# Performance work log

Hardware: AMD Instinct MI355X
Metric: run time of the kernel (lower is better)

The kernel has to match this reference:

```python
import jax, jax.numpy as jnp
import numpy as np

B, T, H = 4096, 2048, 15  # batch, seq_len, n_hidden (hardcoded 15 in module)


def setup_inputs() -> dict:
    key = jax.random.key(0)
    ks = jax.random.split(key, 7)
    s = 1.0 / np.sqrt(H)  # torch default init scale for LSTMCell/Linear
    return {
        "x": jax.random.normal(ks[0], (B, T), dtype=jnp.float32),
        "W_ih": jax.random.uniform(ks[1], (4 * H, 1), jnp.float32, -s, s),
        "W_hh": jax.random.uniform(ks[2], (4 * H, H), jnp.float32, -s, s),
        "b_ih": jax.random.uniform(ks[3], (4 * H,), jnp.float32, -s, s),
        "b_hh": jax.random.uniform(ks[4], (4 * H,), jnp.float32, -s, s),
        "W_lin": jax.random.uniform(ks[5], (1, H), jnp.float32, -s, s),
        "b_lin": jax.random.uniform(ks[6], (1,), jnp.float32, -s, s),
    }


def reference(x, W_ih, W_hh, b_ih, b_hh, W_lin, b_lin):
    # x: [B, T]; one scalar input per timestep (LSTMCell input_size=1).
    b = b_ih + b_hh  # [4H]
    w_ih = W_ih[:, 0]  # [4H] since input_size == 1

    def step(carry, x_t):
        h, c = carry  # [B, H] each
        # gates: [B, 4H], PyTorch gate order i, f, g, o
        gates = x_t[:, None] * w_ih[None, :] + h @ W_hh.T + b
        i_, f_, g_, o_ = jnp.split(gates, 4, axis=1)
        c = jax.nn.sigmoid(f_) * c + jax.nn.sigmoid(i_) * jnp.tanh(g_)
        h = jax.nn.sigmoid(o_) * jnp.tanh(c)
        out = h @ W_lin.T + b_lin  # [B, 1]
        return (h, c), out[:, 0]

    h0 = jnp.zeros((x.shape[0], W_hh.shape[1]), x.dtype)
    c0 = jnp.zeros_like(h0)
    _, outs = jax.lax.scan(step, (h0, c0), x.T)  # outs: [T, B]
    return outs.T  # [B, T], matches torch.cat(outputs, dim=1)
```

## Files before the change

kernel.cpp:

```cpp
#include <hip/hip_runtime.h>


#define HID 15
#define T_LEN 2048
#define B_TOT 4096

template<int CTRL>
__device__ __forceinline__ int dpp_i(int v) {
    return __builtin_amdgcn_update_dpp(0, v, CTRL, 0xF, 0xF, true);
}
template<int CTRL>
__device__ __forceinline__ float dpp_f(float v) {
    return __int_as_float(
        __builtin_amdgcn_update_dpp(0, __float_as_int(v), CTRL, 0xF, 0xF, true));
}

__global__ __launch_bounds__(256) __attribute__((amdgpu_waves_per_eu(1, 1)))
void lstm_seq_kernel(
    const float* __restrict__ x,
    const float* __restrict__ W_ih,
    const float* __restrict__ W_hh,
    const float* __restrict__ b_ih,
    const float* __restrict__ b_hh,
    const float* __restrict__ W_lin,
    const float* __restrict__ b_lin,
    float* __restrict__ out)
{
    const int tid = threadIdx.x;
    const int sub = tid & 15;
    const int u   = (sub < HID) ? sub : (HID - 1);
    const int b   = blockIdx.x * 16 + (tid >> 4);

    int pos[16];
    pos[0]  = sub;
    pos[1]  = dpp_i<0x121>(sub);  pos[2]  = dpp_i<0x122>(sub);
    pos[3]  = dpp_i<0x123>(sub);  pos[4]  = dpp_i<0x124>(sub);
    pos[5]  = dpp_i<0x125>(sub);  pos[6]  = dpp_i<0x126>(sub);
    pos[7]  = dpp_i<0x127>(sub);  pos[8]  = dpp_i<0x128>(sub);
    pos[9]  = dpp_i<0x129>(sub);  pos[10] = dpp_i<0x12A>(sub);
    pos[11] = dpp_i<0x12B>(sub);  pos[12] = dpp_i<0x12C>(sub);
    pos[13] = dpp_i<0x12D>(sub);  pos[14] = dpp_i<0x12E>(sub);
    pos[15] = dpp_i<0x12F>(sub);

    const int r0 = u, r1 = HID + u, r2 = 2 * HID + u, r3 = 3 * HID + u;
    float wg0[16], wg1[16], wg2[16], wg3[16];
#pragma unroll
    for (int j = 0; j < 16; ++j) {
        const int p = pos[j];
        const bool v = (p < HID);
        wg0[j] = v ? W_hh[r0 * HID + p] : 0.0f;
        wg1[j] = v ? W_hh[r1 * HID + p] : 0.0f;
        wg2[j] = v ? W_hh[r2 * HID + p] : 0.0f;
        wg3[j] = v ? W_hh[r3 * HID + p] : 0.0f;
    }
    const float wih0 = W_ih[r0], wih1 = W_ih[r1], wih2 = W_ih[r2], wih3 = W_ih[r3];
    const float bi0 = b_ih[r0] + b_hh[r0];
    const float bi1 = b_ih[r1] + b_hh[r1];
    const float bi2 = b_ih[r2] + b_hh[r2];
    const float bi3 = b_ih[r3] + b_hh[r3];
    const float wlin_m = (sub < HID) ? W_lin[sub] : 0.0f;
    const float blin = b_lin[0];

    const float L  = 1.44269504088896341f;

    float c = 0.0f, hl = 0.0f;
    const float4* __restrict__ x4 = (const float4*)(x + (size_t)b * T_LEN);
    float4* __restrict__ o4       = (float4*)(out + (size_t)b * T_LEN);

    float4 xv = x4[0];
    for (int t0 = 0; t0 < T_LEN / 4; ++t0) {
        const int tn = (t0 + 1 < T_LEN / 4) ? (t0 + 1) : t0;
        const float4 xnext = x4[tn];
        float ov[4];
#pragma unroll
        for (int s = 0; s < 4; ++s) {
            const float xt = (s == 0) ? xv.x : (s == 1) ? xv.y : (s == 2) ? xv.z : xv.w;

            float hr[16];
            hr[0]  = hl;
            hr[1]  = dpp_f<0x121>(hl);  hr[2]  = dpp_f<0x122>(hl);
            hr[3]  = dpp_f<0x123>(hl);  hr[4]  = dpp_f<0x124>(hl);
            hr[5]  = dpp_f<0x125>(hl);  hr[6]  = dpp_f<0x126>(hl);
            hr[7]  = dpp_f<0x127>(hl);  hr[8]  = dpp_f<0x128>(hl);
            hr[9]  = dpp_f<0x129>(hl);  hr[10] = dpp_f<0x12A>(hl);
            hr[11] = dpp_f<0x12B>(hl);  hr[12] = dpp_f<0x12C>(hl);
            hr[13] = dpp_f<0x12D>(hl);  hr[14] = dpp_f<0x12E>(hl);
            hr[15] = dpp_f<0x12F>(hl);

            float a0 = fmaf(xt, wih0, bi0), c0 = 0.0f;
            float a1 = fmaf(xt, wih1, bi1), c1 = 0.0f;
            float a2 = fmaf(xt, wih2, bi2), c2 = 0.0f;
            float a3 = fmaf(xt, wih3, bi3), c3 = 0.0f;
#pragma unroll
            for (int j = 0; j < 16; j += 2) {
                a0 = fmaf(hr[j], wg0[j], a0);  c0 = fmaf(hr[j+1], wg0[j+1], c0);
                a1 = fmaf(hr[j], wg1[j], a1);  c1 = fmaf(hr[j+1], wg1[j+1], c1);
                a2 = fmaf(hr[j], wg2[j], a2);  c2 = fmaf(hr[j+1], wg2[j+1], c2);
                a3 = fmaf(hr[j], wg3[j], a3);  c3 = fmaf(hr[j+1], wg3[j+1], c3);
            }
            const float g0 = a0 + c0;
            const float g1 = a1 + c1;
            const float g2 = a2 + c2;
            const float g3 = a3 + c3;

            const float si = __builtin_amdgcn_rcpf(1.0f + __builtin_amdgcn_exp2f(g0 * -L));
            const float sf = __builtin_amdgcn_rcpf(1.0f + __builtin_amdgcn_exp2f(g1 * -L));
            const float tg = fmaf(2.0f,
                __builtin_amdgcn_rcpf(1.0f + __builtin_amdgcn_exp2f(g2 * (-2.0f * L))), -1.0f);
            const float so = __builtin_amdgcn_rcpf(1.0f + __builtin_amdgcn_exp2f(g3 * -L));

            c = fmaf(sf, c, si * tg);
            const float tc = fmaf(2.0f,
                __builtin_amdgcn_rcpf(1.0f + __builtin_amdgcn_exp2f(c * (-2.0f * L))), -1.0f);
            hl = so * tc;

            float p = hl * wlin_m;
            p += dpp_f<0x0B1>(p);
            p += dpp_f<0x04E>(p);
            p += dpp_f<0x140>(p);
            p += dpp_f<0x141>(p);
            ov[s] = p + blin;
        }
        if (sub == 0) {
            o4[t0] = make_float4(ov[0], ov[1], ov[2], ov[3]);
        }
        xv = xnext;
    }
}

extern "C" void kernel_launch(void* const* d_in, const int* in_sizes, int n_in,
                              void* d_out, int out_size, void* d_ws, size_t ws_size,
                              hipStream_t stream) {
    const float* x     = (const float*)d_in[0];
    const float* W_ih  = (const float*)d_in[1];
    const float* W_hh  = (const float*)d_in[2];
    const float* b_ih  = (const float*)d_in[3];
    const float* b_hh  = (const float*)d_in[4];
    const float* W_lin = (const float*)d_in[5];
    const float* b_lin = (const float*)d_in[6];
    float* out = (float*)d_out;

    dim3 grid(B_TOT / 16);
    dim3 block(256);
    lstm_seq_kernel<<<grid, block, 0, stream>>>(x, W_ih, W_hh, b_ih, b_hh,
                                                W_lin, b_lin, out);
}
```

Baseline: 484.3 us.

## Split LSTM gates across wave halves with packed FMA and permlane32 swap

Each batch row is now spread over 32 lanes instead of 16. The two 32-lane halves each compute two of the four gates, using packed two-wide FMAs, and trade activations with permlane32_swap. The aim is to shorten the serial per-step dependency chain: each lane does half the matvec and transcendental work, and the grid doubles to allow two waves per EU. In exchange it adds cross-half permute latency and duplicated cell/h computation, and it relies on permlane32_swap, which is a gfx950 instruction.

```diff
diff --git a/kernel.cpp b/kernel.cpp
--- a/kernel.cpp
+++ b/kernel.cpp
@@ -4,6 +4,12 @@
 #define HID 15
 #define T_LEN 2048
 #define B_TOT 4096
+
+typedef float v2f __attribute__((ext_vector_type(2)));
+
+__device__ __forceinline__ v2f fma2(v2f a, v2f b, v2f c) {
+    return __builtin_elementwise_fma(a, b, c);
+}
 
 template<int CTRL>
 __device__ __forceinline__ int dpp_i(int v) {
@@ -15,7 +21,7 @@
         __builtin_amdgcn_update_dpp(0, __float_as_int(v), CTRL, 0xF, 0xF, true));
 }
 
-__global__ __launch_bounds__(256) __attribute__((amdgpu_waves_per_eu(1, 1)))
+__global__ __launch_bounds__(256) __attribute__((amdgpu_waves_per_eu(2, 2)))
 void lstm_seq_kernel(
     const float* __restrict__ x,
     const float* __restrict__ W_ih,
@@ -26,10 +32,13 @@
     const float* __restrict__ b_lin,
     float* __restrict__ out)
 {
-    const int tid = threadIdx.x;
-    const int sub = tid & 15;
-    const int u   = (sub < HID) ? sub : (HID - 1);
-    const int b   = blockIdx.x * 16 + (tid >> 4);
+    const int tid  = threadIdx.x;
+    const int lane = tid & 63;
+    const int sub  = tid & 15;
+    const int eidx = (tid >> 4) & 1;
+    const int hf   = (tid >> 5) & 1;
+    const int u    = (sub < HID) ? sub : (HID - 1);
+    const int b    = blockIdx.x * 8 + (tid >> 6) * 2 + eidx;
 
     int pos[16];
     pos[0]  = sub;
@@ -42,28 +51,35 @@
     pos[13] = dpp_i<0x12D>(sub);  pos[14] = dpp_i<0x12E>(sub);
     pos[15] = dpp_i<0x12F>(sub);
 
-    const int r0 = u, r1 = HID + u, r2 = 2 * HID + u, r3 = 3 * HID + u;
-    float wg0[16], wg1[16], wg2[16], wg3[16];
+    auto cal = __builtin_amdgcn_permlane32_swap((unsigned)lane, (unsigned)lane,
+                                                false, false);
+    const bool xlo = ((__builtin_amdgcn_readfirstlane((int)cal[0]) & 32) == 0);
+
+    const int row0 = hf * 2 * HID + u;
+    const int row1 = row0 + HID;
+    v2f wp[16];
 #pragma unroll
     for (int j = 0; j < 16; ++j) {
         const int p = pos[j];
         const bool v = (p < HID);
-        wg0[j] = v ? W_hh[r0 * HID + p] : 0.0f;
-        wg1[j] = v ? W_hh[r1 * HID + p] : 0.0f;
-        wg2[j] = v ? W_hh[r2 * HID + p] : 0.0f;
-        wg3[j] = v ? W_hh[r3 * HID + p] : 0.0f;
+        wp[j].x = v ? W_hh[row0 * HID + p] : 0.0f;
+        wp[j].y = v ? W_hh[row1 * HID + p] : 0.0f;
     }
-    const float wih0 = W_ih[r0], wih1 = W_ih[r1], wih2 = W_ih[r2], wih3 = W_ih[r3];
-    const float bi0 = b_ih[r0] + b_hh[r0];
-    const float bi1 = b_ih[r1] + b_hh[r1];
-    const float bi2 = b_ih[r2] + b_hh[r2];
-    const float bi3 = b_ih[r3] + b_hh[r3];
+    v2f wih; wih.x = W_ih[row0]; wih.y = W_ih[row1];
+    v2f bia; bia.x = b_ih[row0] + b_hh[row0]; bia.y = b_ih[row1] + b_hh[row1];
     const float wlin_m = (sub < HID) ? W_lin[sub] : 0.0f;
     const float blin = b_lin[0];
 
-    const float L  = 1.44269504088896341f;
+    const float L = 1.44269504088896341f;
+    const float m0 = hf ? 2.0f : 1.0f;
+    const float d0 = hf ? -1.0f : 0.0f;
+    v2f sv; sv.x = hf ? (-2.0f * L) : (-L); sv.y = -L;
 
     float c = 0.0f, hl = 0.0f;
+    float hr[16];
+#pragma unroll
+    for (int j = 0; j < 16; ++j) hr[j] = 0.0f;
+
     const float4* __restrict__ x4 = (const float4*)(x + (size_t)b * T_LEN);
     float4* __restrict__ o4       = (float4*)(out + (size_t)b * T_LEN);
 
@@ -76,7 +92,47 @@
         for (int s = 0; s < 4; ++s) {
             const float xt = (s == 0) ? xv.x : (s == 1) ? xv.y : (s == 2) ? xv.z : xv.w;
 
-            float hr[16];
+            v2f ae = bia;
+            v2f ao; ao.x = 0.0f; ao.y = 0.0f;
+#pragma unroll
+            for (int j = 0; j < 16; j += 2) {
+                ae = fma2((v2f){hr[j],     hr[j]},     wp[j],     ae);
+                ao = fma2((v2f){hr[j + 1], hr[j + 1]}, wp[j + 1], ao);
+            }
+            const v2f g = fma2((v2f){xt, xt}, wih, ae + ao);
+
+            const v2f earg = g * sv;
+            const float e0 = __builtin_amdgcn_exp2f(earg.x);
+            const float e1 = __builtin_amdgcn_exp2f(earg.y);
+            const float r0 = __builtin_amdgcn_rcpf(1.0f + e0);
+            const float a1 = __builtin_amdgcn_rcpf(1.0f + e1);
+            const float a0 = fmaf(m0, r0, d0);
+
+            auto ra = __builtin_amdgcn_permlane32_swap(
+                (unsigned)__float_as_int(a0), (unsigned)__float_as_int(a0),
+                false, false);
+            auto rb = __builtin_amdgcn_permlane32_swap(
+                (unsigned)__float_as_int(a1), (unsigned)__float_as_int(a1),
+                false, false);
+            const float prod = __int_as_float((int)ra[0]) * __int_as_float((int)ra[1]);
+            const float rbx = __int_as_float((int)rb[0]);
+            const float rby = __int_as_float((int)rb[1]);
+            const float sfv = xlo ? rbx : rby;
+            const float sov = xlo ? rby : rbx;
+
+            c = fmaf(sfv, c, prod);
+            const float tc = fmaf(2.0f,
+                __builtin_amdgcn_rcpf(1.0f + __builtin_amdgcn_exp2f(c * (-2.0f * L))),
+                -1.0f);
+            hl = sov * tc;
+
+            float p = hl * wlin_m;
+            p += dpp_f<0x0B1>(p);
+            p += dpp_f<0x04E>(p);
+            p += dpp_f<0x140>(p);
+            p += dpp_f<0x141>(p);
+            ov[s] = p + blin;
+
             hr[0]  = hl;
             hr[1]  = dpp_f<0x121>(hl);  hr[2]  = dpp_f<0x122>(hl);
             hr[3]  = dpp_f<0x123>(hl);  hr[4]  = dpp_f<0x124>(hl);
@@ -86,42 +142,8 @@
             hr[11] = dpp_f<0x12B>(hl);  hr[12] = dpp_f<0x12C>(hl);
             hr[13] = dpp_f<0x12D>(hl);  hr[14] = dpp_f<0x12E>(hl);
             hr[15] = dpp_f<0x12F>(hl);
-
-            float a0 = fmaf(xt, wih0, bi0), c0 = 0.0f;
-            float a1 = fmaf(xt, wih1, bi1), c1 = 0.0f;
-            float a2 = fmaf(xt, wih2, bi2), c2 = 0.0f;
-            float a3 = fmaf(xt, wih3, bi3), c3 = 0.0f;
-#pragma unroll
-            for (int j = 0; j < 16; j += 2) {
-                a0 = fmaf(hr[j], wg0[j], a0);  c0 = fmaf(hr[j+1], wg0[j+1], c0);
-                a1 = fmaf(hr[j], wg1[j], a1);  c1 = fmaf(hr[j+1], wg1[j+1], c1);
-                a2 = fmaf(hr[j], wg2[j], a2);  c2 = fmaf(hr[j+1], wg2[j+1], c2);
-                a3 = fmaf(hr[j], wg3[j], a3);  c3 = fmaf(hr[j+1], wg3[j+1], c3);
-            }
-            const float g0 = a0 + c0;
-            const float g1 = a1 + c1;
-            const float g2 = a2 + c2;
-            const float g3 = a3 + c3;
-
-            const float si = __builtin_amdgcn_rcpf(1.0f + __builtin_amdgcn_exp2f(g0 * -L));
-            const float sf = __builtin_amdgcn_rcpf(1.0f + __builtin_amdgcn_exp2f(g1 * -L));
-            const float tg = fmaf(2.0f,
-                __builtin_amdgcn_rcpf(1.0f + __builtin_amdgcn_exp2f(g2 * (-2.0f * L))), -1.0f);
-            const float so = __builtin_amdgcn_rcpf(1.0f + __builtin_amdgcn_exp2f(g3 * -L));
-
-            c = fmaf(sf, c, si * tg);
-            const float tc = fmaf(2.0f,
-                __builtin_amdgcn_rcpf(1.0f + __builtin_amdgcn_exp2f(c * (-2.0f * L))), -1.0f);
-            hl = so * tc;
-
-            float p = hl * wlin_m;
-            p += dpp_f<0x0B1>(p);
-            p += dpp_f<0x04E>(p);
-            p += dpp_f<0x140>(p);
-            p += dpp_f<0x141>(p);
-            ov[s] = p + blin;
         }
-        if (sub == 0) {
+        if (sub == 0 && hf == 0) {
             o4[t0] = make_float4(ov[0], ov[1], ov[2], ov[3]);
         }
         xv = xnext;
@@ -140,7 +162,7 @@
     const float* b_lin = (const float*)d_in[6];
     float* out = (float*)d_out;
 
-    dim3 grid(B_TOT / 16);
+    dim3 grid(B_TOT / 8);
     dim3 block(256);
     lstm_seq_kernel<<<grid, block, 0, stream>>>(x, W_ih, W_hh, b_ih, b_hh,
                                                 W_lin, b_lin, out);
```

Result: slower. 604.2 us (+24.7%).

## Use packed fp16 dot2 for recurrent matvec with prescaled log2e weights

Applied to the files above, without the earlier changes.

Converts the recurrent weights to packed fp16 pairs and computes the 15-wide hidden matvec with v_dot2 instructions. The hidden state is packed once and broadcast with half as many DPP moves. Weights, biases and the cell state are prescaled by -log2e factors so the exp2 arguments need no extra multiplies, and the tanh expressions fold into single FMAs. This shortens the serial per-step critical path, at the cost of fp16 precision in the recurrence, which may accumulate error over 2048 steps.

```diff
diff --git a/kernel.cpp b/kernel.cpp
--- a/kernel.cpp
+++ b/kernel.cpp
@@ -4,6 +4,8 @@
 #define HID 15
 #define T_LEN 2048
 #define B_TOT 4096
+
+typedef __fp16 v2h __attribute__((ext_vector_type(2)));
 
 template<int CTRL>
 __device__ __forceinline__ int dpp_i(int v) {
@@ -13,6 +15,12 @@
 __device__ __forceinline__ float dpp_f(float v) {
     return __int_as_float(
         __builtin_amdgcn_update_dpp(0, __float_as_int(v), CTRL, 0xF, 0xF, true));
+}
+template<int CTRL>
+__device__ __forceinline__ v2h dpp_h(v2h v) {
+    int r = __builtin_amdgcn_update_dpp(0, __builtin_bit_cast(int, v),
+                                        CTRL, 0xF, 0xF, true);
+    return __builtin_bit_cast(v2h, r);
 }
 
 __global__ __launch_bounds__(256) __attribute__((amdgpu_waves_per_eu(1, 1)))
@@ -31,39 +39,50 @@
     const int u   = (sub < HID) ? sub : (HID - 1);
     const int b   = blockIdx.x * 16 + (tid >> 4);
 
+    const int pr0 = sub;
+    const int pr1 = dpp_i<0x121>(sub);
     int pos[16];
-    pos[0]  = sub;
-    pos[1]  = dpp_i<0x121>(sub);  pos[2]  = dpp_i<0x122>(sub);
-    pos[3]  = dpp_i<0x123>(sub);  pos[4]  = dpp_i<0x124>(sub);
-    pos[5]  = dpp_i<0x125>(sub);  pos[6]  = dpp_i<0x126>(sub);
-    pos[7]  = dpp_i<0x127>(sub);  pos[8]  = dpp_i<0x128>(sub);
-    pos[9]  = dpp_i<0x129>(sub);  pos[10] = dpp_i<0x12A>(sub);
-    pos[11] = dpp_i<0x12B>(sub);  pos[12] = dpp_i<0x12C>(sub);
-    pos[13] = dpp_i<0x12D>(sub);  pos[14] = dpp_i<0x12E>(sub);
-    pos[15] = dpp_i<0x12F>(sub);
+    pos[0]  = pr0;                pos[1]  = pr1;
+    pos[2]  = dpp_i<0x122>(pr0);  pos[3]  = dpp_i<0x122>(pr1);
+    pos[4]  = dpp_i<0x124>(pr0);  pos[5]  = dpp_i<0x124>(pr1);
+    pos[6]  = dpp_i<0x126>(pr0);  pos[7]  = dpp_i<0x126>(pr1);
+    pos[8]  = dpp_i<0x128>(pr0);  pos[9]  = dpp_i<0x128>(pr1);
+    pos[10] = dpp_i<0x12A>(pr0);  pos[11] = dpp_i<0x12A>(pr1);
+    pos[12] = dpp_i<0x12C>(pr0);  pos[13] = dpp_i<0x12C>(pr1);
+    pos[14] = dpp_i<0x12E>(pr0);  pos[15] = dpp_i<0x12E>(pr1);
 
+    const double Ld = 1.4426950408889634074;
+    const float  SI = (float)(-Ld);
+    const float  SG = (float)(-2.0 * Ld);
     const int r0 = u, r1 = HID + u, r2 = 2 * HID + u, r3 = 3 * HID + u;
-    float wg0[16], wg1[16], wg2[16], wg3[16];
+    v2h wi[8], wf[8], wg[8], wo[8];
 #pragma unroll
-    for (int j = 0; j < 16; ++j) {
-        const int p = pos[j];
-        const bool v = (p < HID);
-        wg0[j] = v ? W_hh[r0 * HID + p] : 0.0f;
-        wg1[j] = v ? W_hh[r1 * HID + p] : 0.0f;
-        wg2[j] = v ? W_hh[r2 * HID + p] : 0.0f;
-        wg3[j] = v ? W_hh[r3 * HID + p] : 0.0f;
+    for (int j = 0; j < 8; ++j) {
+        const int p0 = pos[2 * j], p1 = pos[2 * j + 1];
+        const bool v0 = (p0 < HID), v1 = (p1 < HID);
+        wi[j].x = (__fp16)(v0 ? W_hh[r0 * HID + p0] * SI : 0.0f);
+        wi[j].y = (__fp16)(v1 ? W_hh[r0 * HID + p1] * SI : 0.0f);
+        wf[j].x = (__fp16)(v0 ? W_hh[r1 * HID + p0] * SI : 0.0f);
+        wf[j].y = (__fp16)(v1 ? W_hh[r1 * HID + p1] * SI : 0.0f);
+        wg[j].x = (__fp16)(v0 ? W_hh[r2 * HID + p0] * SG : 0.0f);
+        wg[j].y = (__fp16)(v1 ? W_hh[r2 * HID + p1] * SG : 0.0f);
+        wo[j].x = (__fp16)(v0 ? W_hh[r3 * HID + p0] * SI : 0.0f);
+        wo[j].y = (__fp16)(v1 ? W_hh[r3 * HID + p1] * SI : 0.0f);
     }
-    const float wih0 = W_ih[r0], wih1 = W_ih[r1], wih2 = W_ih[r2], wih3 = W_ih[r3];
-    const float bi0 = b_ih[r0] + b_hh[r0];
-    const float bi1 = b_ih[r1] + b_hh[r1];
-    const float bi2 = b_ih[r2] + b_hh[r2];
-    const float bi3 = b_ih[r3] + b_hh[r3];
+    const float wih_i = W_ih[r0] * SI, wih_f = W_ih[r1] * SI;
+    const float wih_g = W_ih[r2] * SG, wih_o = W_ih[r3] * SI;
+    const float bia_i = (b_ih[r0] + b_hh[r0]) * SI;
+    const float bia_f = (b_ih[r1] + b_hh[r1]) * SI;
+    const float bia_g = (b_ih[r2] + b_hh[r2]) * SG;
+    const float bia_o = (b_ih[r3] + b_hh[r3]) * SI;
     const float wlin_m = (sub < HID) ? W_lin[sub] : 0.0f;
     const float blin = b_lin[0];
+    const float C4L  = (float)(4.0 * Ld);
+    const float CN2L = (float)(-2.0 * Ld);
 
-    const float L  = 1.44269504088896341f;
+    float cs = 0.0f;
+    float hl = 0.0f;
 
-    float c = 0.0f, hl = 0.0f;
     const float4* __restrict__ x4 = (const float4*)(x + (size_t)b * T_LEN);
     float4* __restrict__ o4       = (float4*)(out + (size_t)b * T_LEN);
 
@@ -76,43 +95,40 @@
         for (int s = 0; s < 4; ++s) {
             const float xt = (s == 0) ? xv.x : (s == 1) ? xv.y : (s == 2) ? xv.z : xv.w;
 
-            float hr[16];
-            hr[0]  = hl;
-            hr[1]  = dpp_f<0x121>(hl);  hr[2]  = dpp_f<0x122>(hl);
-            hr[3]  = dpp_f<0x123>(hl);  hr[4]  = dpp_f<0x124>(hl);
-            hr[5]  = dpp_f<0x125>(hl);  hr[6]  = dpp_f<0x126>(hl);
-            hr[7]  = dpp_f<0x127>(hl);  hr[8]  = dpp_f<0x128>(hl);
-            hr[9]  = dpp_f<0x129>(hl);  hr[10] = dpp_f<0x12A>(hl);
-            hr[11] = dpp_f<0x12B>(hl);  hr[12] = dpp_f<0x12C>(hl);
-            hr[13] = dpp_f<0x12D>(hl);  hr[14] = dpp_f<0x12E>(hl);
-            hr[15] = dpp_f<0x12F>(hl);
+            const float h1 = dpp_f<0x121>(hl);
+            v2h pk[8];
+            pk[0] = __builtin_amdgcn_cvt_pkrtz(hl, h1);
+            pk[1] = dpp_h<0x122>(pk[0]);
+            pk[2] = dpp_h<0x124>(pk[0]);
+            pk[3] = dpp_h<0x126>(pk[0]);
+            pk[4] = dpp_h<0x128>(pk[0]);
+            pk[5] = dpp_h<0x12A>(pk[0]);
+            pk[6] = dpp_h<0x12C>(pk[0]);
+            pk[7] = dpp_h<0x12E>(pk[0]);
 
-            float a0 = fmaf(xt, wih0, bi0), c0 = 0.0f;
-            float a1 = fmaf(xt, wih1, bi1), c1 = 0.0f;
-            float a2 = fmaf(xt, wih2, bi2), c2 = 0.0f;
-            float a3 = fmaf(xt, wih3, bi3), c3 = 0.0f;
+            float ai = bia_i, af = bia_f, ag = bia_g, aq = bia_o;
 #pragma unroll
-            for (int j = 0; j < 16; j += 2) {
-                a0 = fmaf(hr[j], wg0[j], a0);  c0 = fmaf(hr[j+1], wg0[j+1], c0);
-                a1 = fmaf(hr[j], wg1[j], a1);  c1 = fmaf(hr[j+1], wg1[j+1], c1);
-                a2 = fmaf(hr[j], wg2[j], a2);  c2 = fmaf(hr[j+1], wg2[j+1], c2);
-                a3 = fmaf(hr[j], wg3[j], a3);  c3 = fmaf(hr[j+1], wg3[j+1], c3);
+            for (int j = 0; j < 8; ++j) {
+                ai = __builtin_amdgcn_fdot2(pk[j], wi[j], ai, false);
+                af = __builtin_amdgcn_fdot2(pk[j], wf[j], af, false);
+                ag = __builtin_amdgcn_fdot2(pk[j], wg[j], ag, false);
+                aq = __builtin_amdgcn_fdot2(pk[j], wo[j], aq, false);
             }
-            const float g0 = a0 + c0;
-            const float g1 = a1 + c1;
-            const float g2 = a2 + c2;
-            const float g3 = a3 + c3;
+            const float gi = fmaf(xt, wih_i, ai);
+            const float gf = fmaf(xt, wih_f, af);
+            const float gg = fmaf(xt, wih_g, ag);
+            const float go = fmaf(xt, wih_o, aq);
 
-            const float si = __builtin_amdgcn_rcpf(1.0f + __builtin_amdgcn_exp2f(g0 * -L));
-            const float sf = __builtin_amdgcn_rcpf(1.0f + __builtin_amdgcn_exp2f(g1 * -L));
-            const float tg = fmaf(2.0f,
-                __builtin_amdgcn_rcpf(1.0f + __builtin_amdgcn_exp2f(g2 * (-2.0f * L))), -1.0f);
-            const float so = __builtin_amdgcn_rcpf(1.0f + __builtin_amdgcn_exp2f(g3 * -L));
+            const float si = __builtin_amdgcn_rcpf(1.0f + __builtin_amdgcn_exp2f(gi));
+            const float sf = __builtin_amdgcn_rcpf(1.0f + __builtin_amdgcn_exp2f(gf));
+            const float rg = __builtin_amdgcn_rcpf(1.0f + __builtin_amdgcn_exp2f(gg));
+            const float so = __builtin_amdgcn_rcpf(1.0f + __builtin_amdgcn_exp2f(go));
+            const float tg2 = fmaf(C4L, rg, CN2L);
 
-            c = fmaf(sf, c, si * tg);
-            const float tc = fmaf(2.0f,
-                __builtin_amdgcn_rcpf(1.0f + __builtin_amdgcn_exp2f(c * (-2.0f * L))), -1.0f);
-            hl = so * tc;
+            cs = fmaf(sf, cs, si * tg2);
+            const float rc = __builtin_amdgcn_rcpf(1.0f + __builtin_amdgcn_exp2f(-cs));
+            const float tso = so + so;
+            hl = fmaf(tso, rc, -so);
 
             float p = hl * wlin_m;
             p += dpp_f<0x0B1>(p);
```

Result: faster. 413.8 us (-14.6%).
